# Kernel tuning notes

Hardware: AMD Instinct MI355X
Metric: run time of the kernel (lower is better)

## Reference

```python
import math
import jax, jax.numpy as jnp
import numpy as np

C, H, W = 128, 64, 64
R, K = 7, 3          # 7x3 dilated window
PAD_H, PAD_W = 9, 2  # from unfold paddings
DIL_H, DIL_W = 3, 2  # row/col dilations


def _neighborhood(x):
    """Gather dilated 7x3 neighborhood: out[n,c,r,k,i,j] = x[n,c, i+3r-9, j+2k-2] (zero-padded).
    x: (n,c,h,w) -> (n,c,7,3,h,w)."""
    n, c, h, w = x.shape
    xp = jnp.pad(x, ((0, 0), (0, 0), (PAD_H, PAD_H), (PAD_W, PAD_W)))
    taps = [xp[:, :, DIL_H * r:DIL_H * r + h, DIL_W * k:DIL_W * k + w]
            for r in range(R) for k in range(K)]
    return jnp.stack(taps, axis=2).reshape(n, c, R, K, h, w)


def setup_inputs() -> dict:
    key = jax.random.key(0)
    k1, k2, k3 = jax.random.split(key, 3)
    x = jax.random.normal(k1, (4, C, H, W), dtype=jnp.float32)
    p5_w = 0.1 * jax.random.normal(k2, (1, C, R, K, H, W), dtype=jnp.float32)
    p6_w = 0.1 * jax.random.normal(k3, (1, C, R, K, C), dtype=jnp.float32)
    return {"x": x, "p5_w": p5_w, "p6_w": p6_w}


def reference(x, p5_w, p6_w):
    n, c, h, w = x.shape
    # t_2: dilated 7x3 neighborhood gather (double unfold)
    t2 = _neighborhood(x)                                   # (n,c,7,3,h,w)
    # t_3: bmm((n,c*21,hw), (n,hw,c)) / sqrt(hw)
    t3 = jnp.einsum('ncrkhw,ndhw->ncrkd', t2, x) / math.sqrt(h * w)  # (n,c,7,3,c)
    # elementwise modulation
    t7 = p5_w * t2 + t2                                     # (n,c,7,3,h,w)
    t6 = p6_w * t3                                          # (n,c,7,3,c)
    # t_8: bmm((n,hw,c*21), (n,c*21,c)) / sqrt(c*21)
    t8 = jnp.einsum('ncrkhw,ncrkd->nhwd', t7, t6) / math.sqrt(c * R * K)  # (n,h,w,c)
    return jnp.transpose(t8, (0, 3, 1, 2))                  # (n,c,h,w)
```

## Files before the change

### kernel.cpp

```cpp
#include <hip/hip_runtime.h>

typedef _Float16 f16;
typedef _Float16 f16x2 __attribute__((ext_vector_type(2)));
typedef _Float16 f16x4 __attribute__((ext_vector_type(4)));
typedef _Float16 f16x8 __attribute__((ext_vector_type(8)));
typedef float    f32x4 __attribute__((ext_vector_type(4)));

#define XROWS 82
#define XSTR  (XROWS * 64)
#define XK_ELEMS (3u * 4u * 128u * (unsigned)XSTR)
static const size_t T6T_OFF   = (size_t)XK_ELEMS * 2;
static const size_t T6T_BYTES = (size_t)4 * 128 * 2688 * 2;
static const size_t T3P_OFF   = T6T_OFF + T6T_BYTES;
static const size_t T8P_OFF   = T3P_OFF;

__device__ __forceinline__ void gl16(const f16* g, f16* l) {
  __builtin_amdgcn_global_load_lds((const __attribute__((address_space(1))) void*)g,
                                   (__attribute__((address_space(3))) void*)l, 16, 0, 0);
}

__global__ __launch_bounds__(256) void prep_kernel(const float* __restrict__ x,
                                                   f16* __restrict__ xk) {
  unsigned p = blockIdx.x * 256u + threadIdx.x;
  unsigned rest = p / 656u;
  unsigned q    = p - rest * 656u;
  unsigned row  = q >> 3;
  unsigned wp   = q & 7u;
  unsigned c    = rest & 127u;
  unsigned n    = (rest >> 7) & 3u;
  unsigned kc   = rest >> 9;

  int hsrc = (int)row - 9;
  f16x8 v = {};
  if (hsrc >= 0 && hsrc < 64) {
    const float* base = x + (((size_t)(n * 128u + c) * 64u + (unsigned)hsrc) * 64u);
    int w0 = (int)(wp * 8u) + 2 * (int)kc - 2;
#pragma unroll
    for (int i = 0; i < 8; i++) {
      int wsrc = w0 + i;
      v[i] = (wsrc >= 0 && wsrc < 64) ? (f16)(base[wsrc] * 0.125f) : (f16)0.f;
    }
  }
  ((f16x8*)xk)[p] = v;
}

__global__ __launch_bounds__(256, 3) void gram_kernel(const f16* __restrict__ xk,
                                                      f16* __restrict__ t3p) {
  __shared__ f16 gl[2 * 12288];

  unsigned b    = blockIdx.x;
  unsigned ks   = b & 7u;
  unsigned cseg = (b >> 3) & 1u;
  unsigned rki  = (b >> 4) % 11u;
  unsigned n    = b / 176u;
  unsigned r    = rki / 3u;
  unsigned kc   = rki - r * 3u;

  unsigned tid  = threadIdx.x;
  unsigned wv   = tid >> 6;
  unsigned lane = tid & 63u;
  unsigned wy   = wv >> 1;
  unsigned wx   = wv & 1u;
  unsigned quad = lane >> 4;
  unsigned l16  = lane & 15u;
  unsigned rsl  = lane >> 3;
  unsigned seg  = (lane & 7u) ^ (rsl & 7u);

  unsigned h0 = ks * 8u;
  const f16* Ab = xk + (size_t)(kc * 4u + n) * 128u * XSTR + (size_t)(cseg * 64u) * XSTR
                + (h0 + 3u * r) * 64u + seg * 8u;
  const f16* Bb = xk + (size_t)(4u + n) * 128u * XSTR + (h0 + 9u) * 64u + seg * 8u;
  unsigned ar0 = wv * 16u;
  unsigned br0 = wv * 32u;

  f32x4 acc[2][4] = {};

#pragma unroll
  for (unsigned t = 0; t < 2u; t++)
    gl16(Ab + (size_t)(ar0 + t * 8u + rsl) * XSTR, &gl[(ar0 + t * 8u) * 64u]);
#pragma unroll
  for (unsigned t = 0; t < 4u; t++)
    gl16(Bb + (size_t)(br0 + t * 8u + rsl) * XSTR, &gl[4096u + (br0 + t * 8u) * 64u]);

  for (unsigned s = 0; s < 8u; s++) {
    __syncthreads();
    if (s < 7u) {
      f16* base = &gl[((s + 1u) & 1u) * 12288u];
      unsigned off = (s + 1u) * 64u;
#pragma unroll
      for (unsigned t = 0; t < 2u; t++)
        gl16(Ab + off + (size_t)(ar0 + t * 8u + rsl) * XSTR, base + (ar0 + t * 8u) * 64u);
#pragma unroll
      for (unsigned t = 0; t < 4u; t++)
        gl16(Bb + off + (size_t)(br0 + t * 8u + rsl) * XSTR, base + 4096u + (br0 + t * 8u) * 64u);
    }
    const f16* bufA = &gl[(s & 1u) * 12288u];
    const f16* bufB = bufA + 4096u;
#pragma unroll
    for (unsigned t2 = 0; t2 < 2u; t2++) {
      unsigned L = t2 * 4u + quad;
      f16x8 a[2], bb[4];
#pragma unroll
      for (int ms = 0; ms < 2; ms++) {
        unsigned rr = wy * 32u + (unsigned)ms * 16u + l16;
        a[ms] = *(const f16x8*)&bufA[rr * 64u + (L ^ (rr & 7u)) * 8u];
      }
#pragma unroll
      for (int ns = 0; ns < 4; ns++) {
        unsigned rb = wx * 64u + (unsigned)ns * 16u + l16;
        bb[ns] = *(const f16x8*)&bufB[rb * 64u + (L ^ (rb & 7u)) * 8u];
      }
#pragma unroll
      for (int ms = 0; ms < 2; ms++)
#pragma unroll
        for (int ns = 0; ns < 4; ns++)
          acc[ms][ns] = __builtin_amdgcn_mfma_f32_16x16x32_f16(a[ms], bb[ns], acc[ms][ns], 0, 0, 0);
    }
  }

  f16* tp = t3p + ((size_t)(ks * 4u + n) * 11u + rki) * 16384u;
#pragma unroll
  for (int ms = 0; ms < 2; ms++) {
#pragma unroll
    for (int ns = 0; ns < 4; ns++) {
      unsigned c0 = cseg * 64u + wy * 32u + (unsigned)ms * 16u + quad * 4u;
      unsigned d  = wx * 64u + (unsigned)ns * 16u + l16;
#pragma unroll
      for (int reg = 0; reg < 4; reg++)
        tp[(size_t)(c0 + (unsigned)reg) * 128u + d] = (f16)acc[ms][ns][reg];
    }
  }
}

__global__ __launch_bounds__(256) void ep_kernel(const f16* __restrict__ t3p,
                                                 const float* __restrict__ p6,
                                                 f16* __restrict__ t6T) {
  unsigned idx = blockIdx.x * 256u + threadIdx.x;
  unsigned t   = idx >> 12;
  unsigned rk  = t % 21u;
  unsigned n   = t / 21u;

  if (rk <= 10u) {
    unsigned d4 = idx & 31u;
    unsigned c  = (idx >> 5) & 127u;
    unsigned d0 = d4 * 4u;
    float s0 = 0.f, s1 = 0.f, s2 = 0.f, s3 = 0.f;
#pragma unroll
    for (unsigned ks = 0; ks < 8u; ks++) {
      f16x4 v = *(const f16x4*)(t3p + (((size_t)(ks * 4u + n) * 11u + rk) * 16384u + c * 128u + d0));
      s0 += (float)v[0]; s1 += (float)v[1]; s2 += (float)v[2]; s3 += (float)v[3];
    }
    const float* pp = p6 + ((size_t)c * 21u + rk) * 128u + d0;
    f16* ob = t6T + (size_t)(n * 128u + d0) * 2688u + rk * 128u + c;
    ob[0]        = (f16)(s0 * pp[0]);
    ob[2688]     = (f16)(s1 * pp[1]);
    ob[2 * 2688] = (f16)(s2 * pp[2]);
    ob[3 * 2688] = (f16)(s3 * pp[3]);
  } else {
    unsigned mrk = 20u - rk;
    unsigned c4 = idx & 31u;
    unsigned d  = (idx >> 5) & 127u;
    unsigned c0 = c4 * 4u;
    float s0 = 0.f, s1 = 0.f, s2 = 0.f, s3 = 0.f;
#pragma unroll
    for (unsigned ks = 0; ks < 8u; ks++) {
      f16x4 v = *(const f16x4*)(t3p + (((size_t)(ks * 4u + n) * 11u + mrk) * 16384u + d * 128u + c0));
      s0 += (float)v[0]; s1 += (float)v[1]; s2 += (float)v[2]; s3 += (float)v[3];
    }
    f16x4 o;
    o[0] = (f16)(s0 * p6[((size_t)(c0 + 0u) * 21u + rk) * 128u + d]);
    o[1] = (f16)(s1 * p6[((size_t)(c0 + 1u) * 21u + rk) * 128u + d]);
    o[2] = (f16)(s2 * p6[((size_t)(c0 + 2u) * 21u + rk) * 128u + d]);
    o[3] = (f16)(s3 * p6[((size_t)(c0 + 3u) * 21u + rk) * 128u + d]);
    *(f16x4*)(t6T + (size_t)(n * 128u + d) * 2688u + rk * 128u + c0) = o;
  }
}

#define ALDS_STR 40
#define RT_STR   72
__global__ __launch_bounds__(256, 4) void outp_kernel(const f16* __restrict__ xk,
                                                      const float* __restrict__ p5,
                                                      const f16* __restrict__ t6T,
                                                      f16* __restrict__ t8p) {
  __shared__ f16 smem[128 * RT_STR];
  f16* Alds = smem;

  unsigned b = blockIdx.x;
  unsigned g = b & 3u;
  unsigned h = (b >> 2) & 63u;
  unsigned n = b >> 8;

  unsigned tid  = threadIdx.x;
  unsigned wv   = tid >> 6;
  unsigned lane = tid & 63u;
  unsigned wy   = wv >> 1;
  unsigned wx   = wv & 1u;
  unsigned quad = lane >> 4;
  unsigned l16  = lane & 15u;
  unsigned wst  = tid & 63u;
  unsigned g8   = tid >> 6;

  unsigned cbase = g * 32u + g8 * 8u;
  const float* prow0 = p5 + (size_t)cbase * (21u * 4096u) + h * 64u + wst;
  const f16* bfb = t6T + (size_t)(n * 128u + wx * 64u + l16) * 2688u + g * 32u + quad * 8u;

  f32x4 acc[2][4] = {};
  f16 xv[8]; float pv[8];
  f16x8 bfc[4];

  {
    const f16* xrow = xk + (((size_t)n * 128u + cbase) * XROWS + h) * 64u + wst;
#pragma unroll
    for (int i = 0; i < 8; i++) { xv[i] = xrow[(size_t)i * XSTR]; pv[i] = prow0[(size_t)i * (21u * 4096u)]; }
#pragma unroll
    for (int ns = 0; ns < 4; ns++) bfc[ns] = *(const f16x8*)(bfb + (size_t)ns * 16u * 2688u);
  }

  for (unsigned j = 0; j < 21u; j++) {
    f16* Ag = Alds + (j & 1u) * 2560u;
    {
      f16x8 av;
#pragma unroll
      for (int i = 0; i < 8; i++) av[i] = (f16)((float)xv[i] * (1.0f + pv[i]));
      *(f16x8*)&Ag[wst * ALDS_STR + g8 * 8u] = av;
    }
    __syncthreads();

    f16x8 bfn[4];
    if (j < 20u) {
      unsigned rk = j + 1u;
      unsigned rr = rk / 3u;
      unsigned kcc = rk - rr * 3u;
      const f16* xrow = xk + (((size_t)(kcc * 4u + n) * 128u + cbase) * XROWS + (h + 3u * rr)) * 64u + wst;
      const float* prow = prow0 + rk * 4096u;
#pragma unroll
      for (int i = 0; i < 8; i++) { xv[i] = xrow[(size_t)i * XSTR]; pv[i] = prow[(size_t)i * (21u * 4096u)]; }
#pragma unroll
      for (int ns = 0; ns < 4; ns++) bfn[ns] = *(const f16x8*)(bfb + (size_t)ns * 16u * 2688u + rk * 128u);
    }

    f16x8 a[2];
#pragma unroll
    for (int ms = 0; ms < 2; ms++)
      a[ms] = *(const f16x8*)&Ag[(wy * 32u + (unsigned)ms * 16u + l16) * ALDS_STR + quad * 8u];
#pragma unroll
    for (int ms = 0; ms < 2; ms++)
#pragma unroll
      for (int ns = 0; ns < 4; ns++)
        acc[ms][ns] = __builtin_amdgcn_mfma_f32_16x16x32_f16(a[ms], bfc[ns], acc[ms][ns], 0, 0, 0);
#pragma unroll
    for (int ns = 0; ns < 4; ns++) bfc[ns] = bfn[ns];
  }

  __syncthreads();
  f16* Rt = smem;
#pragma unroll
  for (int ms = 0; ms < 2; ms++)
#pragma unroll
    for (int ns = 0; ns < 4; ns++) {
      unsigned w0 = wy * 32u + (unsigned)ms * 16u + quad * 4u;
      unsigned d  = wx * 64u + (unsigned)ns * 16u + l16;
      f16x4 t;
#pragma unroll
      for (int reg = 0; reg < 4; reg++) t[reg] = (f16)acc[ms][ns][reg];
      *(f16x4*)&Rt[d * RT_STR + w0] = t;
    }
  __syncthreads();
  f16* op = t8p + ((size_t)((g * 4u + n) * 64u + h)) * 8192u;
#pragma unroll
  for (unsigned it = 0; it < 4u; it++) {
    unsigned row = (tid >> 3) + it * 32u;
    unsigned w0  = (tid & 7u) * 8u;
    f16x8 o = *(const f16x8*)&Rt[row * RT_STR + w0];
    *(f16x8*)(op + row * 64u + w0) = o;
  }
}

__global__ __launch_bounds__(256) void red_kernel(const f16* __restrict__ t8p,
                                                  float* __restrict__ out) {
  unsigned idx = blockIdx.x * 256u + threadIdx.x;
  unsigned w0 = (idx & 7u) * 8u;
  unsigned h  = (idx >> 3) & 63u;
  unsigned d  = (idx >> 9) & 127u;
  unsigned n  = idx >> 16;
  const float FS = 0.15430334996209192f;
  float s[8] = {};
#pragma unroll
  for (unsigned g = 0; g < 4u; g++) {
    f16x8 v = *(const f16x8*)(t8p + ((size_t)((g * 4u + n) * 64u + h)) * 8192u + d * 64u + w0);
#pragma unroll
    for (int i = 0; i < 8; i++) s[i] += (float)v[i];
  }
  f32x4 o0, o1;
#pragma unroll
  for (int i = 0; i < 4; i++) { o0[i] = s[i] * FS; o1[i] = s[i + 4] * FS; }
  float* op = out + ((size_t)(n * 128u + d) * 64u + h) * 64u + w0;
  *(f32x4*)op = o0;
  *(f32x4*)(op + 4) = o1;
}

extern "C" void kernel_launch(void* const* d_in, const int* in_sizes, int n_in,
                              void* d_out, int out_size, void* d_ws, size_t ws_size,
                              hipStream_t stream) {
  const float* x  = (const float*)d_in[0];
  const float* p5 = (const float*)d_in[1];
  const float* p6 = (const float*)d_in[2];
  float* out = (float*)d_out;
  f16* xk  = (f16*)((char*)d_ws);
  f16* t6T = (f16*)((char*)d_ws + T6T_OFF);
  f16* t3p = (f16*)((char*)d_ws + T3P_OFF);
  f16* t8p = (f16*)((char*)d_ws + T8P_OFF);

  hipLaunchKernelGGL(prep_kernel, dim3(3936), dim3(256), 0, stream, x, xk);
  hipLaunchKernelGGL(gram_kernel, dim3(704),  dim3(256), 0, stream, xk, t3p);
  hipLaunchKernelGGL(ep_kernel,   dim3(1344), dim3(256), 0, stream, t3p, p6, t6T);
  hipLaunchKernelGGL(outp_kernel, dim3(1024), dim3(256), 0, stream, xk, p5, t6T, t8p);
  hipLaunchKernelGGL(red_kernel,  dim3(1024), dim3(256), 0, stream, t8p, out);
}
```

Measured before the change: 176.9 us.

## Pre-transpose x taps and p5 into channel-contiguous fp16 layouts for outp

A new prepX kernel writes both the existing per-tap xk layout and a transposed xkT layout, in which 32 channels per width position are contiguous, using an LDS transpose. A new prepPQ kernel converts p5 into a transposed fp16 tensor holding 1+p5. outp_kernel can then load 8 channels with one vector load each for x and the modulation, and does the multiply in packed fp16 instead of issuing strided scalar loads. The cost is an extra prep kernel that reads all of p5 every call and writes about 38 MB more of workspace, and the modulation is now computed in fp16.

```diff
diff --git a/kernel.cpp b/kernel.cpp
--- a/kernel.cpp
+++ b/kernel.cpp
@@ -8,40 +8,96 @@
 
 #define XROWS 82
 #define XSTR  (XROWS * 64)
-#define XK_ELEMS (3u * 4u * 128u * (unsigned)XSTR)
-static const size_t T6T_OFF   = (size_t)XK_ELEMS * 2;
-static const size_t T6T_BYTES = (size_t)4 * 128 * 2688 * 2;
-static const size_t T3P_OFF   = T6T_OFF + T6T_BYTES;
-static const size_t T8P_OFF   = T3P_OFF;
+static const size_t XK_OFF  = 0;
+static const size_t XKT_OFF = 16121856;
+static const size_t Q5T_OFF = XKT_OFF + 16121856;
+static const size_t T6T_OFF = Q5T_OFF + 22020096;
+static const size_t T3P_OFF = T6T_OFF + 2752512;
+static const size_t T8P_OFF = T3P_OFF;
 
 __device__ __forceinline__ void gl16(const f16* g, f16* l) {
   __builtin_amdgcn_global_load_lds((const __attribute__((address_space(1))) void*)g,
                                    (__attribute__((address_space(3))) void*)l, 16, 0, 0);
 }
 
-__global__ __launch_bounds__(256) void prep_kernel(const float* __restrict__ x,
-                                                   f16* __restrict__ xk) {
-  unsigned p = blockIdx.x * 256u + threadIdx.x;
-  unsigned rest = p / 656u;
-  unsigned q    = p - rest * 656u;
-  unsigned row  = q >> 3;
-  unsigned wp   = q & 7u;
-  unsigned c    = rest & 127u;
-  unsigned n    = (rest >> 7) & 3u;
-  unsigned kc   = rest >> 9;
-
+__global__ __launch_bounds__(256) void prepX_kernel(const float* __restrict__ x,
+                                                    f16* __restrict__ xkT,
+                                                    f16* __restrict__ xk) {
+  __shared__ float T[128][65];
+  unsigned b   = blockIdx.x;
+  unsigned row = b % 82u;
+  unsigned t2_ = b / 82u;
+  unsigned n   = t2_ & 3u;
+  unsigned kc  = t2_ >> 2;
   int hsrc = (int)row - 9;
-  f16x8 v = {};
+  unsigned tid = threadIdx.x;
+  unsigned w = tid & 63u, g = tid >> 6;
+  f16* oT = xkT + (((size_t)(g * 3u + kc) * 4u + n) * 82u + row) * 2048u;
+  f16* oX = xk + ((size_t)(kc * 4u + n) * 128u + (tid >> 1)) * XSTR + row * 64u + (tid & 1u) * 32u;
+
   if (hsrc >= 0 && hsrc < 64) {
-    const float* base = x + (((size_t)(n * 128u + c) * 64u + (unsigned)hsrc) * 64u);
-    int w0 = (int)(wp * 8u) + 2 * (int)kc - 2;
+    unsigned c = tid >> 1, half = (tid & 1u) * 32u;
+    const float* src = x + ((size_t)(n * 128u + c) * 64u + (unsigned)hsrc) * 64u + half;
 #pragma unroll
     for (int i = 0; i < 8; i++) {
-      int wsrc = w0 + i;
-      v[i] = (wsrc >= 0 && wsrc < 64) ? (f16)(base[wsrc] * 0.125f) : (f16)0.f;
-    }
-  }
-  ((f16x8*)xk)[p] = v;
+      f32x4 v = *(const f32x4*)(src + i * 4);
+      *(f32x4*)&T[c][half + (unsigned)i * 4u] = v;
+    }
+    __syncthreads();
+    int wsrc = (int)w + 2 * (int)kc - 2;
+    bool ok = (wsrc >= 0 && wsrc < 64);
+#pragma unroll
+    for (unsigned s = 0; s < 4u; s++) {
+      f16x8 o;
+#pragma unroll
+      for (int i = 0; i < 8; i++)
+        o[i] = ok ? (f16)(T[g * 32u + s * 8u + (unsigned)i][wsrc] * 0.125f) : (f16)0.f;
+      *(f16x8*)(oT + w * 32u + s * 8u) = o;
+    }
+#pragma unroll
+    for (unsigned s = 0; s < 4u; s++) {
+      f16x8 o;
+#pragma unroll
+      for (int i = 0; i < 8; i++) {
+        int ws = (int)(half + s * 8u + (unsigned)i) + 2 * (int)kc - 2;
+        o[i] = (ws >= 0 && ws < 64) ? (f16)(T[c][ws] * 0.125f) : (f16)0.f;
+      }
+      *(f16x8*)(oX + s * 8u) = o;
+    }
+  } else {
+    f16x8 z = {};
+#pragma unroll
+    for (unsigned s = 0; s < 4u; s++) *(f16x8*)(oT + w * 32u + s * 8u) = z;
+#pragma unroll
+    for (unsigned s = 0; s < 4u; s++) *(f16x8*)(oX + s * 8u) = z;
+  }
+}
+
+__global__ __launch_bounds__(256) void prepPQ_kernel(const float* __restrict__ p5,
+                                                     f16* __restrict__ q5T) {
+  __shared__ float T[128][65];
+  unsigned b  = blockIdx.x;
+  unsigned h  = b & 63u;
+  unsigned rk = b >> 6;
+  unsigned tid = threadIdx.x;
+  unsigned c = tid >> 1, half = (tid & 1u) * 32u;
+  const float* src = p5 + ((size_t)c * 21u + rk) * 4096u + h * 64u + half;
+#pragma unroll
+  for (int i = 0; i < 8; i++) {
+    f32x4 v = *(const f32x4*)(src + i * 4);
+    *(f32x4*)&T[c][half + (unsigned)i * 4u] = v;
+  }
+  __syncthreads();
+  unsigned w = tid & 63u, g = tid >> 6;
+  f16* oplane = q5T + ((size_t)(g * 21u + rk) * 64u + h) * 2048u;
+#pragma unroll
+  for (unsigned s = 0; s < 4u; s++) {
+    f16x8 o;
+#pragma unroll
+    for (int i = 0; i < 8; i++)
+      o[i] = (f16)(1.0f + T[g * 32u + s * 8u + (unsigned)i][w]);
+    *(f16x8*)(oplane + w * 32u + s * 8u) = o;
+  }
 }
 
 __global__ __launch_bounds__(256, 3) void gram_kernel(const f16* __restrict__ xk,
@@ -178,8 +234,8 @@
 
 #define ALDS_STR 40
 #define RT_STR   72
-__global__ __launch_bounds__(256, 4) void outp_kernel(const f16* __restrict__ xk,
-                                                      const float* __restrict__ p5,
+__global__ __launch_bounds__(256, 4) void outp_kernel(const f16* __restrict__ xkT,
+                                                      const f16* __restrict__ q5T,
                                                       const f16* __restrict__ t6T,
                                                       f16* __restrict__ t8p) {
   __shared__ f16 smem[128 * RT_STR];
@@ -197,21 +253,20 @@
   unsigned wx   = wv & 1u;
   unsigned quad = lane >> 4;
   unsigned l16  = lane & 15u;
-  unsigned wst  = tid & 63u;
-  unsigned g8   = tid >> 6;
-
-  unsigned cbase = g * 32u + g8 * 8u;
-  const float* prow0 = p5 + (size_t)cbase * (21u * 4096u) + h * 64u + wst;
+  unsigned sw   = tid >> 2;
+  unsigned sc   = tid & 3u;
+  unsigned soff = sw * 32u + sc * 8u;
+
+  const f16* xgb = xkT + (size_t)(g * 3u) * 4u * 82u * 2048u;
+  const f16* qgb = q5T + (size_t)(g * 21u) * 64u * 2048u + (size_t)h * 2048u;
   const f16* bfb = t6T + (size_t)(n * 128u + wx * 64u + l16) * 2688u + g * 32u + quad * 8u;
 
   f32x4 acc[2][4] = {};
-  f16 xv[8]; float pv[8];
-  f16x8 bfc[4];
+  f16x8 xa, qa, bfc[4];
 
   {
-    const f16* xrow = xk + (((size_t)n * 128u + cbase) * XROWS + h) * 64u + wst;
-#pragma unroll
-    for (int i = 0; i < 8; i++) { xv[i] = xrow[(size_t)i * XSTR]; pv[i] = prow0[(size_t)i * (21u * 4096u)]; }
+    xa = *(const f16x8*)(xgb + ((size_t)(0u * 4u + n) * 82u + h) * 2048u + soff);
+    qa = *(const f16x8*)(qgb + soff);
 #pragma unroll
     for (int ns = 0; ns < 4; ns++) bfc[ns] = *(const f16x8*)(bfb + (size_t)ns * 16u * 2688u);
   }
@@ -219,22 +274,18 @@
   for (unsigned j = 0; j < 21u; j++) {
     f16* Ag = Alds + (j & 1u) * 2560u;
     {
-      f16x8 av;
-#pragma unroll
-      for (int i = 0; i < 8; i++) av[i] = (f16)((float)xv[i] * (1.0f + pv[i]));
-      *(f16x8*)&Ag[wst * ALDS_STR + g8 * 8u] = av;
+      f16x8 av = xa * qa;
+      *(f16x8*)&Ag[sw * ALDS_STR + sc * 8u] = av;
     }
     __syncthreads();
 
-    f16x8 bfn[4];
+    f16x8 xan, qan, bfn[4];
     if (j < 20u) {
       unsigned rk = j + 1u;
       unsigned rr = rk / 3u;
       unsigned kcc = rk - rr * 3u;
-      const f16* xrow = xk + (((size_t)(kcc * 4u + n) * 128u + cbase) * XROWS + (h + 3u * rr)) * 64u + wst;
-      const float* prow = prow0 + rk * 4096u;
-#pragma unroll
-      for (int i = 0; i < 8; i++) { xv[i] = xrow[(size_t)i * XSTR]; pv[i] = prow[(size_t)i * (21u * 4096u)]; }
+      xan = *(const f16x8*)(xgb + ((size_t)(kcc * 4u + n) * 82u + h + 3u * rr) * 2048u + soff);
+      qan = *(const f16x8*)(qgb + (size_t)rk * 64u * 2048u + soff);
 #pragma unroll
       for (int ns = 0; ns < 4; ns++) bfn[ns] = *(const f16x8*)(bfb + (size_t)ns * 16u * 2688u + rk * 128u);
     }
@@ -248,6 +299,7 @@
 #pragma unroll
       for (int ns = 0; ns < 4; ns++)
         acc[ms][ns] = __builtin_amdgcn_mfma_f32_16x16x32_f16(a[ms], bfc[ns], acc[ms][ns], 0, 0, 0);
+    xa = xan; qa = qan;
 #pragma unroll
     for (int ns = 0; ns < 4; ns++) bfc[ns] = bfn[ns];
   }
@@ -306,14 +358,17 @@
   const float* p5 = (const float*)d_in[1];
   const float* p6 = (const float*)d_in[2];
   float* out = (float*)d_out;
-  f16* xk  = (f16*)((char*)d_ws);
+  f16* xk  = (f16*)((char*)d_ws + XK_OFF);
+  f16* xkT = (f16*)((char*)d_ws + XKT_OFF);
+  f16* q5T = (f16*)((char*)d_ws + Q5T_OFF);
   f16* t6T = (f16*)((char*)d_ws + T6T_OFF);
   f16* t3p = (f16*)((char*)d_ws + T3P_OFF);
   f16* t8p = (f16*)((char*)d_ws + T8P_OFF);
 
-  hipLaunchKernelGGL(prep_kernel, dim3(3936), dim3(256), 0, stream, x, xk);
-  hipLaunchKernelGGL(gram_kernel, dim3(704),  dim3(256), 0, stream, xk, t3p);
-  hipLaunchKernelGGL(ep_kernel,   dim3(1344), dim3(256), 0, stream, t3p, p6, t6T);
-  hipLaunchKernelGGL(outp_kernel, dim3(1024), dim3(256), 0, stream, xk, p5, t6T, t8p);
-  hipLaunchKernelGGL(red_kernel,  dim3(1024), dim3(256), 0, stream, t8p, out);
-}
+  hipLaunchKernelGGL(prepX_kernel,  dim3(984),  dim3(256), 0, stream, x, xkT, xk);
+  hipLaunchKernelGGL(prepPQ_kernel, dim3(1344), dim3(256), 0, stream, p5, q5T);
+  hipLaunchKernelGGL(gram_kernel,   dim3(704),  dim3(256), 0, stream, xk, t3p);
+  hipLaunchKernelGGL(ep_kernel,     dim3(1344), dim3(256), 0, stream, t3p, p6, t6T);
+  hipLaunchKernelGGL(outp_kernel,   dim3(1024), dim3(256), 0, stream, xkT, q5T, t6T, t8p);
+  hipLaunchKernelGGL(red_kernel,    dim3(1024), dim3(256), 0, stream, t8p, out);
+}
```

After: 179.3 us. No clear change (+1.3%).
